# Optimization experiments

Hardware: AMD Instinct MI355X
Metric: run time of the kernel (lower is better)

The kernel has to match this reference:

```python
import jax, jax.numpy as jnp
import numpy as np

B, T, C_IN, H, W = 4, 3, 64, 64, 64
E = 96            # embed_dim
K = 3             # patch_size / deformable kernel size
PAD = 1
N = K * K         # 9 sampled positions per pixel
TOPK = 2
DG = 8            # deformable groups


def conv3x3(x, w, b):
    y = jax.lax.conv_general_dilated(x, w, (1, 1), ((1, 1), (1, 1)),
                                     dimension_numbers=('NCHW', 'OIHW', 'NCHW'))
    return y + b[None, :, None, None]


def lrelu(x):
    return jnp.where(x >= 0, x, 0.1 * x)


def deform_sample(x, off_feat, om_w, om_b):
    """DSP_sep2: modulated deformable sampling. Returns (B, C, N, H, W)."""
    B_, C, H_, W_ = x.shape
    om = conv3x3(off_feat, om_w, om_b).reshape(B_, 3, DG, N, H_, W_)
    off_y, off_x, mask = om[:, 0], om[:, 1], jax.nn.sigmoid(om[:, 2])  # (B,DG,N,H,W)
    ky = (jnp.arange(N) // K - PAD).astype(x.dtype)
    kx = (jnp.arange(N) % K - PAD).astype(x.dtype)
    py = off_y + ky[None, None, :, None, None] + jnp.arange(H_, dtype=x.dtype)[None, None, None, :, None]
    px = off_x + kx[None, None, :, None, None] + jnp.arange(W_, dtype=x.dtype)[None, None, None, None, :]
    y0 = jnp.floor(py); x0 = jnp.floor(px)
    wy = py - y0;       wx = px - x0
    xg = x.reshape(B_, DG, C // DG, H_, W_)
    gat = jax.vmap(jax.vmap(lambda xg_, yi, xi: xg_[:, yi, xi]))  # -> (B,DG,Cg,N,H,W)

    def corner(yc, xc, wgt):
        valid = ((yc >= 0) & (yc < H_) & (xc >= 0) & (xc < W_)).astype(x.dtype)
        yi = jnp.clip(yc, 0, H_ - 1).astype(jnp.int32)
        xi = jnp.clip(xc, 0, W_ - 1).astype(jnp.int32)
        return gat(xg, yi, xi) * (wgt * valid)[:, :, None]

    out = (corner(y0,     x0,     (1 - wy) * (1 - wx)) +
           corner(y0,     x0 + 1, (1 - wy) * wx) +
           corner(y0 + 1, x0,     wy * (1 - wx)) +
           corner(y0 + 1, x0 + 1, wy * wx))
    out = out * mask[:, :, None]  # modulation
    return out.reshape(B_, C, N, H_, W_)


def deform_attn(q, k, v, oc1_w, oc1_b, oc2_w, oc2_b, om_w, om_b):
    B_, E_, H_, W_ = q.shape
    HW = H_ * W_
    off = lrelu(conv3x3(jnp.concatenate([q, k], axis=1), oc1_w, oc1_b))
    off = lrelu(conv3x3(off, oc2_w, oc2_b))
    ko = deform_sample(k, off, om_w, om_b).transpose(0, 3, 4, 2, 1).reshape(B_, HW, N, E_)
    vo = deform_sample(v, off, om_w, om_b).transpose(0, 3, 4, 2, 1).reshape(B_, HW, N, E_)
    qr = q.reshape(B_, E_, HW).transpose(0, 2, 1)              # (B,HW,E)
    rel = jnp.einsum('bpne,bpe->bpn', ko, qr)                  # (B,HW,N)
    vals, idx = jax.lax.top_k(rel, TOPK)                       # (B,HW,k)
    corr = jax.nn.softmax(vals, axis=-1)
    idx_e = jnp.broadcast_to(idx[..., None], idx.shape + (E_,))
    ksel = jnp.take_along_axis(ko, idx_e, axis=2)              # (B,HW,k,E)
    vsel = jnp.take_along_axis(vo, idx_e, axis=2)
    k_up = jnp.einsum('bpke,bpk->bpe', ksel, corr)
    w_ori = jnp.einsum('bpe,bpe->bp', qr, k_up)                # (B,HW)
    v_re = jnp.einsum('bpke,bpk->bpe', vsel, corr).transpose(0, 2, 1)  # (B,E,HW)
    return w_ori, v_re


def setup_inputs() -> dict:
    key = jax.random.key(0)
    ks = jax.random.split(key, 18)
    s = 0.05
    return {
        'fea_full_map': jax.random.normal(ks[0], (B, T, C_IN, H, W), jnp.float32),
        'cf_w': s * jax.random.normal(ks[1], (E, C_IN, 3, 3), jnp.float32),
        'cf_b': s * jax.random.normal(ks[2], (E,), jnp.float32),
        'wq':   s * jax.random.normal(ks[3], (E, E), jnp.float32),
        'bq':   s * jax.random.normal(ks[4], (E,), jnp.float32),
        'wk':   s * jax.random.normal(ks[5], (E, E), jnp.float32),
        'bk':   s * jax.random.normal(ks[6], (E,), jnp.float32),
        'wv':   s * jax.random.normal(ks[7], (E, E), jnp.float32),
        'bv':   s * jax.random.normal(ks[8], (E,), jnp.float32),
        'oc1_w': s * jax.random.normal(ks[9], (E, 2 * E, 3, 3), jnp.float32),
        'oc1_b': s * jax.random.normal(ks[10], (E,), jnp.float32),
        'oc2_w': s * jax.random.normal(ks[11], (E, E, 3, 3), jnp.float32),
        'oc2_b': s * jax.random.normal(ks[12], (E,), jnp.float32),
        'om_w': 0.01 * jax.random.normal(ks[13], (DG * 3 * N, E, 3, 3), jnp.float32),
        'om_b': 0.01 * jax.random.normal(ks[14], (DG * 3 * N,), jnp.float32),
        'cl_w': s * jax.random.normal(ks[15], (C_IN, E, 3, 3), jnp.float32),
        'cl_b': s * jax.random.normal(ks[16], (C_IN,), jnp.float32),
    }


def reference(fea_full_map, cf_w, cf_b, wq, bq, wk, bk, wv, bv,
              oc1_w, oc1_b, oc2_w, oc2_b, om_w, om_b, cl_w, cl_b):
    B_, T_, C_, H_, W_ = fea_full_map.shape
    x = fea_full_map.reshape(B_ * T_, C_, H_, W_)
    emb = conv3x3(x, cf_w, cf_b).reshape(B_, T_, E, H_, W_)
    # per-frame linear Q/K/V over the channel dim (nn.Linear: y = x W^T + b)
    q = jnp.einsum('btchw,dc->btdhw', emb, wq) + bq[None, None, :, None, None]
    k = jnp.einsum('btchw,dc->btdhw', emb, wk) + bk[None, None, :, None, None]
    v = jnp.einsum('btchw,dc->btdhw', emb, wv) + bv[None, None, :, None, None]
    feats = []
    for jj in range(T_):
        ws, vs = [], []
        for ii in range(T_):
            if ii != jj:
                w_, v_ = deform_attn(q[:, jj], k[:, ii], v[:, ii],
                                     oc1_w, oc1_b, oc2_w, oc2_b, om_w, om_b)
                ws.append(w_); vs.append(v_)
        wm = jax.nn.softmax(jnp.stack(ws, axis=1), axis=1)  # (B, T-1, HW)
        vm = jnp.stack(vs, axis=1)                          # (B, T-1, E, HW)
        feats.append((vm * wm[:, :, None, :]).sum(axis=1).reshape(B_, E, H_, W_))
    f = jnp.stack(feats, axis=1).reshape(B_ * T_, E, H_, W_)
    out = conv3x3(f, cl_w, cl_b)
    return out + x
```

## Files before the change

kernel.cpp:

```cpp
#include <hip/hip_runtime.h>
#include <math.h>

#define PIXN 4096

typedef _Float16 f16;
typedef short s16x8 __attribute__((ext_vector_type(8)));
typedef unsigned short u16x4 __attribute__((ext_vector_type(4)));
typedef float f32x4 __attribute__((ext_vector_type(4)));

__device__ __forceinline__ f16 f2h(float f) { return (f16)f; }
__device__ __forceinline__ float h2f(f16 h) { return (float)h; }

__device__ __forceinline__ unsigned short f2bf(float f) {
  unsigned u = __float_as_uint(f);
  u += 0x7fffu + ((u >> 16) & 1u);
  return (unsigned short)(u >> 16);
}
__device__ __forceinline__ float bf2f(unsigned short h) {
  return __uint_as_float(((unsigned)h) << 16);
}

enum { ACT_NONE = 0, ACT_LRELU = 1, ACT_SIG144 = 2 };
enum { IN_FLAT = 1, IN_UVPAIR = 2, IN_QKV = 3, IN_BF = 4, IN_MERGE = 5 };
enum { OUT_FLAT = 0, OUT_NCHWRES = 1, OUT_BF = 2 };

__device__ __forceinline__ void wprep_mfma(const float* __restrict__ w, unsigned short* __restrict__ dst,
                                           int srcCIN, int cinOff, int COUTv, int COUTP,
                                           int total, int idx) {
  if (idx >= total) return;
  int e = idx & 7;
  int t = idx >> 3;
  int co = t % COUTP; t /= COUTP;
  int kch = t & 3; t >>= 2;
  int kc = t % 3;
  int tap = t / 3;
  int ci = kc * 32 + kch * 8 + e;
  float v = 0.f;
  if (co < COUTv) v = w[((long)co * srcCIN + cinOff + ci) * 9 + tap];
  unsigned short h = f2bf(v);
  dst[idx] = h;
  dst[total + idx] = f2bf(v - bf2f(h));
}

__global__ __launch_bounds__(256) void prep_all(
    const float* __restrict__ cf_w, const float* __restrict__ oc1_w,
    const float* __restrict__ oc2_w, const float* __restrict__ om_w,
    const float* __restrict__ cl_w,
    const float* __restrict__ wq, const float* __restrict__ wk, const float* __restrict__ wv,
    const float* __restrict__ bq, const float* __restrict__ bk, const float* __restrict__ bv,
    const float* __restrict__ cf_b,
    unsigned short* __restrict__ WBQ, float* __restrict__ BQ,
    unsigned short* __restrict__ WB1, unsigned short* __restrict__ WB2,
    unsigned short* __restrict__ WB3, unsigned short* __restrict__ WB4) {
  int idx = blockIdx.x * 256 + threadIdx.x;
  switch (blockIdx.y) {
    case 0: {
      if (idx < 288) {
        int m = idx / 96, ep = idx % 96;
        const float* wm = (m == 0) ? wq : (m == 1) ? wk : wv;
        const float* bm = (m == 0) ? bq : (m == 1) ? bk : bv;
        float s = bm[ep];
        for (int c = 0; c < 96; ++c) s = fmaf(wm[ep * 96 + c], cf_b[c], s);
        BQ[idx] = s;
      }
      if (idx < 165888) {
        int e = idx & 7;
        int t = idx >> 3;
        int co = t % 288; t /= 288;
        int kch = t & 3; t >>= 2;
        int kc = t & 1, tap = t >> 1;
        int ci = kc * 32 + kch * 8 + e;
        int m = co / 96, ep = co % 96;
        const float* wm = (m == 0) ? wq : (m == 1) ? wk : wv;
        float s = 0.f;
        for (int c = 0; c < 96; ++c)
          s = fmaf(wm[ep * 96 + c], cf_w[((long)c * 64 + ci) * 9 + tap], s);
        unsigned short h = f2bf(s);
        WBQ[idx] = h;
        WBQ[165888 + idx] = f2bf(s - bf2f(h));
      }
      break;
    }
    case 1: wprep_mfma(oc1_w, WB1, 192, 0, 96, 96, 82944, idx); break;
    case 2: wprep_mfma(oc1_w, WB1 + 2 * 82944, 192, 96, 96, 96, 82944, idx); break;
    case 3: wprep_mfma(oc2_w, WB2, 96, 0, 96, 96, 82944, idx); break;
    case 4: wprep_mfma(om_w, WB3, 96, 0, 216, 256, 221184, idx); break;
    default: wprep_mfma(cl_w, WB4, 96, 0, 64, 64, 55296, idx); break;
  }
}

__global__ __launch_bounds__(256) void nchw2bf(const float* __restrict__ fea,
                                               unsigned short* __restrict__ hi,
                                               unsigned short* __restrict__ lo) {
  const int y = blockIdx.x;
  const int img = blockIdx.y;
  const int t = threadIdx.x;
  const int x = t & 63, cg = t >> 6;
  __shared__ unsigned short sh[64][68], sl[64][68];
  const float* base = fea + ((long)img * 64) * PIXN + y * 64;
#pragma unroll
  for (int k = 0; k < 16; ++k) {
    int ci = cg * 16 + k;
    float v = base[(long)ci * PIXN + x];
    unsigned short h = f2bf(v);
    sh[x][ci] = h;
    sl[x][ci] = f2bf(v - bf2f(h));
  }
  __syncthreads();
  const long ob = (long)img * PIXN + y * 64;
  for (int i = t; i < 2048; i += 256) {
    int plane = i >> 10;
    int r = i & 1023;
    int px = r >> 4, q4 = r & 15;
    u16x4 v4 = *reinterpret_cast<const u16x4*>(plane ? &sl[px][q4 * 4] : &sh[px][q4 * 4]);
    unsigned short* dst = (plane ? lo : hi) + (ob + px) * 64 + q4 * 4;
    *reinterpret_cast<u16x4*>(dst) = v4;
  }
}

template <int CIN, int COUT, int COUTW, int NCOG, int IMODE, int ACT, int OMODE, int WN>
__global__ __launch_bounds__(512, 4) void conv3x3r(
    const float* __restrict__ in, const float* __restrict__ in2,
    const float* __restrict__ bias_in,
    const unsigned short* __restrict__ WB,
    const float* __restrict__ bias,
    float* __restrict__ out,
    const float* __restrict__ resid) {
  constexpr int KC = CIN / 32;
  constexpr int WM = 8 / WN;
  constexpr int MT = WN;
  constexpr int COG = COUTW / NCOG;
  constexpr int NTW = COG / (WN * 16);
  constexpr int AST = 4 * 66 * 8 + 8;
  constexpr int APL = 4 * AST;
  constexpr int BSTEP = COUTW * 32;
  constexpr int TOTB = 9 * KC * BSTEP;

  __shared__ __align__(16) unsigned short Abuf[2 * APL];
  __shared__ float s_sm[(IMODE == IN_MERGE) ? 528 : 4];

  const int tid = threadIdx.x;
  const int lane = tid & 63;
  const int wid = tid >> 6;
  const int wm = wid % WM;
  const int wn = wid / WM;
  const int iz = blockIdx.y;
  const int y0 = blockIdx.x * 2;
  const int zoff = (NCOG > 1) ? blockIdx.z * COG : 0;

  const float* baseA = nullptr;
  const float* baseB2 = nullptr;
  const unsigned short* hpl = nullptr;
  const unsigned short* lpl = nullptr;
  const unsigned short* wbe = WB;
  int LDV = CIN;
  if constexpr (IMODE == IN_UVPAIR) {
    int pair = iz >> 2, b = iz & 3;
    int jj = pair >> 1, rr2 = pair & 1;
    int ii = (rr2 == 0) ? (jj == 0 ? 1 : 0) : (jj == 2 ? 1 : 2);
    baseA = in + (long)(b * 3 + jj) * (PIXN * 96);
    baseB2 = in2 + (long)(b * 3 + ii) * (PIXN * 96);
    LDV = 96;
  } else if constexpr (IMODE == IN_QKV) {
    int sel = iz / 12, img = iz % 12;
    baseA = in + (long)img * (PIXN * 288) + sel * 96;
    wbe = WB + (long)sel * (2 * TOTB);
    LDV = 288;
  } else if constexpr (IMODE == IN_BF) {
    hpl = reinterpret_cast<const unsigned short*>(in) + (long)iz * ((long)PIXN * CIN);
    lpl = reinterpret_cast<const unsigned short*>(in2) + (long)iz * ((long)PIXN * CIN);
  } else if constexpr (IMODE == IN_MERGE) {
  } else {
    baseA = in + (long)iz * ((long)PIXN * CIN);
    LDV = CIN;
  }

  auto stageA = [&](int kc) {
    if constexpr (IMODE == IN_BF) {
      for (int i = tid; i < 4 * 66 * 4; i += 512) {
        int ci8 = i & 3;
        int t = i >> 2;
        int xp = t % 66, rr = t / 66;
        int y = y0 + rr - 1, x = xp - 1;
        s16x8 hv = {0, 0, 0, 0, 0, 0, 0, 0};
        s16x8 lv = {0, 0, 0, 0, 0, 0, 0, 0};
        if ((unsigned)y < 64u && (unsigned)x < 64u) {
          long off = (long)(y * 64 + x) * CIN + kc * 32 + ci8 * 8;
          hv = *reinterpret_cast<const s16x8*>(hpl + off);
          lv = *reinterpret_cast<const s16x8*>(lpl + off);
        }
        int base = ci8 * AST + (rr * 66 + xp) * 8;
        *reinterpret_cast<s16x8*>(&Abuf[base]) = hv;
        *reinterpret_cast<s16x8*>(&Abuf[APL + base]) = lv;
      }
    } else if constexpr (IMODE == IN_MERGE) {
      const f16* vrep = reinterpret_cast<const f16*>(in);
      const int bb = iz / 3, jjm = iz % 3;
      const int pr0 = jjm * 2;
      for (int i = tid; i < 4 * 66 * 8; i += 512) {
        int ci4 = i & 7;
        int t = i >> 3;
        int xp = t % 66, rr = t / 66;
        int y = y0 + rr - 1, x = xp - 1;
        float4 v = make_float4(0.f, 0.f, 0.f, 0.f);
        if ((unsigned)y < 64u && (unsigned)x < 64u) {
          long bpi = (long)bb * PIXN + y * 64 + x;
          float s0 = s_sm[t * 2], s1 = s_sm[t * 2 + 1];
          const f16* pa = vrep + ((long)pr0 * 16384 + bpi) * 96 + kc * 32 + ci4 * 4;
          const f16* pb = vrep + ((long)(pr0 + 1) * 16384 + bpi) * 96 + kc * 32 + ci4 * 4;
          v.x = s0 * h2f(pa[0]) + s1 * h2f(pb[0]);
          v.y = s0 * h2f(pa[1]) + s1 * h2f(pb[1]);
          v.z = s0 * h2f(pa[2]) + s1 * h2f(pb[2]);
          v.w = s0 * h2f(pa[3]) + s1 * h2f(pb[3]);
        }
        unsigned short h0 = f2bf(v.x), h1 = f2bf(v.y), h2 = f2bf(v.z), h3 = f2bf(v.w);
        u16x4 hv = {h0, h1, h2, h3};
        u16x4 lv = {f2bf(v.x - bf2f(h0)), f2bf(v.y - bf2f(h1)),
                    f2bf(v.z - bf2f(h2)), f2bf(v.w - bf2f(h3))};
        int base = (ci4 >> 1) * AST + (rr * 66 + xp) * 8 + (ci4 & 1) * 4;
        *reinterpret_cast<u16x4*>(&Abuf[base]) = hv;
        *reinterpret_cast<u16x4*>(&Abuf[APL + base]) = lv;
      }
    } else {
      for (int i = tid; i < 4 * 66 * 8; i += 512) {
        int ci4 = i & 7;
        int t = i >> 3;
        int xp = t % 66, rr = t / 66;
        int y = y0 + rr - 1, x = xp - 1;
        float4 v = make_float4(0.f, 0.f, 0.f, 0.f);
        if ((unsigned)y < 64u && (unsigned)x < 64u) {
          long off = (long)(y * 64 + x) * LDV + kc * 32 + ci4 * 4;
          if constexpr (IMODE == IN_UVPAIR) {
            float4 u = *reinterpret_cast<const float4*>(baseA + off);
            float4 w2 = *reinterpret_cast<const float4*>(baseB2 + off);
            float4 bi = *reinterpret_cast<const float4*>(bias_in + kc * 32 + ci4 * 4);
            v.x = u.x + w2.x + bi.x; v.x = v.x >= 0.f ? v.x : 0.1f * v.x;
            v.y = u.y + w2.y + bi.y; v.y = v.y >= 0.f ? v.y : 0.1f * v.y;
            v.z = u.z + w2.z + bi.z; v.z = v.z >= 0.f ? v.z : 0.1f * v.z;
            v.w = u.w + w2.w + bi.w; v.w = v.w >= 0.f ? v.w : 0.1f * v.w;
          } else {
            v = *reinterpret_cast<const float4*>(baseA + off);
          }
        }
        unsigned short h0 = f2bf(v.x), h1 = f2bf(v.y), h2 = f2bf(v.z), h3 = f2bf(v.w);
        u16x4 hv = {h0, h1, h2, h3};
        u16x4 lv = {f2bf(v.x - bf2f(h0)), f2bf(v.y - bf2f(h1)),
                    f2bf(v.z - bf2f(h2)), f2bf(v.w - bf2f(h3))};
        int base = (ci4 >> 1) * AST + (rr * 66 + xp) * 8 + (ci4 & 1) * 4;
        *reinterpret_cast<u16x4*>(&Abuf[base]) = hv;
        *reinterpret_cast<u16x4*>(&Abuf[APL + base]) = lv;
      }
    }
  };

  f32x4 acc[MT][NTW];
#pragma unroll
  for (int nt = 0; nt < NTW; ++nt) {
    int co = zoff + (wn * NTW + nt) * 16 + (lane & 15);
    float b0 = 0.f;
    if (bias != nullptr && co < COUT) b0 = bias[co];
#pragma unroll
    for (int mt = 0; mt < MT; ++mt) {
      acc[mt][nt][0] = b0; acc[mt][nt][1] = b0;
      acc[mt][nt][2] = b0; acc[mt][nt][3] = b0;
    }
  }

  if constexpr (IMODE == IN_MERGE) {
    const float* wbp = in2;
    const int bb = iz / 3, jjm = iz % 3;
    const int pr0 = jjm * 2;
    for (int t = tid; t < 264; t += 512) {
      int rr = t / 66, xp = t - rr * 66;
      int y = y0 + rr - 1, x = xp - 1;
      float s0 = 0.f, s1 = 0.f;
      if ((unsigned)y < 64u && (unsigned)x < 64u) {
        long bpi = (long)bb * PIXN + y * 64 + x;
        float w0 = wbp[(long)pr0 * 16384 + bpi];
        float w1 = wbp[(long)(pr0 + 1) * 16384 + bpi];
        float mx = fmaxf(w0, w1);
        float e0 = expf(w0 - mx), e1 = expf(w1 - mx);
        float inv = 1.f / (e0 + e1);
        s0 = e0 * inv; s1 = e1 * inv;
      }
      s_sm[t * 2] = s0; s_sm[t * 2 + 1] = s1;
    }
    __syncthreads();
  }

  stageA(0);
  __syncthreads();

  const int blo = ((lane >> 4) * COUTW + zoff + (wn * NTW) * 16 + (lane & 15)) * 8;

  s16x8 cbh[NTW], cbl[NTW], pbh[NTW], pbl[NTW];
#pragma unroll
  for (int nt = 0; nt < NTW; ++nt) {
    const unsigned short* p = wbe + (long)nt * 128 + blo;
    pbh[nt] = *reinterpret_cast<const s16x8*>(p);
    pbl[nt] = *reinterpret_cast<const s16x8*>(p + TOTB);
  }

  long bo = 0;
#pragma unroll 1
  for (int kc = 0; kc < KC; ++kc) {
#pragma unroll 1
    for (int tap = 0; tap < 9; ++tap) {
      const int dy = tap / 3, dx = tap % 3;
      const bool last = (kc == KC - 1) && (tap == 8);
      const long bo_next = (tap < 8) ? bo + (long)KC * BSTEP : (long)(kc + 1) * BSTEP;

#pragma unroll
      for (int nt = 0; nt < NTW; ++nt) { cbh[nt] = pbh[nt]; cbl[nt] = pbl[nt]; }
      if (!last) {
#pragma unroll
        for (int nt = 0; nt < NTW; ++nt) {
          const unsigned short* np = wbe + bo_next + (long)nt * 128 + blo;
          pbh[nt] = *reinterpret_cast<const s16x8*>(np);
          pbl[nt] = *reinterpret_cast<const s16x8*>(np + TOTB);
        }
      }

      s16x8 ah[MT], al[MT];
      {
        int ci8 = lane >> 4;
        int m = lane & 15;
#pragma unroll
        for (int mt = 0; mt < MT; ++mt) {
          int px = (wm * MT + mt) * 16 + m;
          int r = px >> 6, x = px & 63;
          int aoff = ci8 * AST + ((r + dy) * 66 + (x + dx)) * 8;
          ah[mt] = *reinterpret_cast<const s16x8*>(&Abuf[aoff]);
          al[mt] = *reinterpret_cast<const s16x8*>(&Abuf[APL + aoff]);
        }
      }

#pragma unroll
      for (int nt = 0; nt < NTW; ++nt) {
#pragma unroll
        for (int mt = 0; mt < MT; ++mt) {
          acc[mt][nt] = __builtin_amdgcn_mfma_f32_16x16x32_bf16(ah[mt], cbh[nt], acc[mt][nt], 0, 0, 0);
          acc[mt][nt] = __builtin_amdgcn_mfma_f32_16x16x32_bf16(al[mt], cbh[nt], acc[mt][nt], 0, 0, 0);
          acc[mt][nt] = __builtin_amdgcn_mfma_f32_16x16x32_bf16(ah[mt], cbl[nt], acc[mt][nt], 0, 0, 0);
        }
      }
      bo = bo_next;
    }
    if (kc + 1 < KC) {
      __syncthreads();
      stageA(kc + 1);
      __syncthreads();
    }
  }

#pragma unroll
  for (int mt = 0; mt < MT; ++mt) {
#pragma unroll
    for (int nt = 0; nt < NTW; ++nt) {
      int co = zoff + (wn * NTW + nt) * 16 + (lane & 15);
      if (COUTW > COUT && co >= COUT) continue;
#pragma unroll
      for (int r = 0; r < 4; ++r) {
        int px = (wm * MT + mt) * 16 + (lane >> 4) * 4 + r;
        float v = acc[mt][nt][r];
        if constexpr (ACT == ACT_LRELU) v = v >= 0.f ? v : 0.1f * v;
        if constexpr (ACT == ACT_SIG144) {
          if (co >= 144) v = 1.f / (1.f + expf(-v));
        }
        if constexpr (OMODE == OUT_FLAT) {
          const long obase = (long)iz * PIXN + blockIdx.x * 128;
          out[(obase + px) * COUT + co] = v;
        } else if constexpr (OMODE == OUT_BF) {
          unsigned short* outh = reinterpret_cast<unsigned short*>(out);
          const long plane = (long)gridDim.y * PIXN * COUT;
          const long obase = (long)iz * PIXN + blockIdx.x * 128;
          long oidx = (obase + px) * COUT + co;
          unsigned short h = f2bf(v);
          outh[oidx] = h;
          outh[plane + oidx] = f2bf(v - bf2f(h));
        } else {
          long oo = (long)iz * ((long)COUT * PIXN) + (long)co * PIXN + blockIdx.x * 128 + px;
          out[oo] = v + resid[oo];
        }
      }
    }
  }
}

#define CWSLOT 580
__global__ __launch_bounds__(256) void attn3_k(const float* __restrict__ qkv,
                                               const float* __restrict__ om,
                                               float* __restrict__ w_buf,
                                               f16* __restrict__ vre) {
  const int pair = blockIdx.y;
  const int jj = pair >> 1, rr = pair & 1;
  const int ii = (rr == 0) ? (jj == 0 ? 1 : 0) : (jj == 2 ? 1 : 2);
  const int wv = threadIdx.x >> 6;
  const int lane = threadIdx.x & 63;
  const int bp0 = blockIdx.x * 8 + wv * 2;

  __shared__ float s_om[8 * 216];
  __shared__ float s_cw[8 * CWSLOT];

  {
    const float* omrow = om + ((long)pair * 16384 + bp0) * 216;
    float* dst = s_om + wv * 432;
    for (int i = lane; i < 432; i += 64) dst[i] = omrow[i];
  }
  __syncthreads();

  for (int t = lane; t < 144; t += 64) {
    int ph = t / 72, cmb = t - ph * 72;
    int g = cmb / 9, n = cmb - g * 9;
    int p = (bp0 + ph) & 4095;
    int y = p >> 6, x = p & 63;
    const float* so = s_om + (wv * 2 + ph) * 216;
    float oy = so[g * 9 + n], ox = so[72 + g * 9 + n], m = so[144 + g * 9 + n];
    float py = oy + (float)(y + n / 3 - 1);
    float px = ox + (float)(x + n % 3 - 1);
    float y0f = floorf(py), x0f = floorf(px);
    float wy = py - y0f, wx = px - x0f;
    float* dst = s_cw + (wv * 2 + ph) * CWSLOT + cmb * 8;
#pragma unroll
    for (int dy = 0; dy < 2; ++dy) {
#pragma unroll
      for (int dx = 0; dx < 2; ++dx) {
        float yc = y0f + dy, xc = x0f + dx;
        bool valid = (yc >= 0.f) & (yc < 64.f) & (xc >= 0.f) & (xc < 64.f);
        float w = (dy ? wy : 1.f - wy) * (dx ? wx : 1.f - wx) * m;
        w = valid ? w : 0.f;
        int yi = (int)fminf(fmaxf(yc, 0.f), 63.f);
        int xi = (int)fminf(fmaxf(xc, 0.f), 63.f);
        int idx = (yi * 64 + xi) * 288 + 96;
        dst[dy * 2 + dx] = w;
        dst[4 + dy * 2 + dx] = __int_as_float(idx);
      }
    }
  }
  __syncthreads();

  const int ph = lane >> 5;
  const int li = lane & 31;
  const int bp = bp0 + ph;
  const int b = bp >> 12;
  const int cb = li * 3;
  const int g = li >> 2;
  const float* kimg = qkv + (long)(b * 3 + ii) * (PIXN * 288);
  const float* qrow = qkv + ((long)(b * 3 + jj) * PIXN + (bp & 4095)) * 288 + cb;
  const float q0 = qrow[0], q1 = qrow[1], q2 = qrow[2];
  const float* cw = s_cw + (wv * 2 + ph) * CWSLOT + g * 9 * 8;

  float ka[9][3];
  float rel[9];
#pragma unroll
  for (int n = 0; n < 9; ++n) {
    float4 w4 = *reinterpret_cast<const float4*>(cw + n * 8);
    float4 i4 = *reinterpret_cast<const float4*>(cw + n * 8 + 4);
    int ia = __float_as_int(i4.x) + cb, ib = __float_as_int(i4.y) + cb;
    int ic = __float_as_int(i4.z) + cb, id = __float_as_int(i4.w) + cb;
#pragma unroll
    for (int j = 0; j < 3; ++j) {
      float a = w4.x * kimg[ia + j];
      a = fmaf(w4.y, kimg[ib + j], a);
      a = fmaf(w4.z, kimg[ic + j], a);
      a = fmaf(w4.w, kimg[id + j], a);
      ka[n][j] = a;
    }
    float part = q0 * ka[n][0];
    part = fmaf(q1, ka[n][1], part);
    part = fmaf(q2, ka[n][2], part);
#pragma unroll
    for (int off = 16; off > 0; off >>= 1) part += __shfl_xor(part, off, 64);
    rel[n] = part;
  }

  int i0 = 0; float v0 = rel[0];
  float ks0a = ka[0][0], ks0b = ka[0][1], ks0c = ka[0][2];
#pragma unroll
  for (int n = 1; n < 9; ++n) {
    bool t = rel[n] > v0;
    v0 = t ? rel[n] : v0; i0 = t ? n : i0;
    ks0a = t ? ka[n][0] : ks0a; ks0b = t ? ka[n][1] : ks0b; ks0c = t ? ka[n][2] : ks0c;
  }
  int i1 = 0; float v1 = -3.4e38f;
  float ks1a = 0.f, ks1b = 0.f, ks1c = 0.f;
#pragma unroll
  for (int n = 0; n < 9; ++n) {
    bool t = (n != i0) && rel[n] > v1;
    v1 = t ? rel[n] : v1; i1 = t ? n : i1;
    ks1a = t ? ka[n][0] : ks1a; ks1b = t ? ka[n][1] : ks1b; ks1c = t ? ka[n][2] : ks1c;
  }
  float e = expf(v1 - v0);
  float cw0 = 1.f / (1.f + e), cw1 = e * cw0;

  float wpart = q0 * (cw0 * ks0a + cw1 * ks1a);
  wpart = fmaf(q1, cw0 * ks0b + cw1 * ks1b, wpart);
  wpart = fmaf(q2, cw0 * ks0c + cw1 * ks1c, wpart);
#pragma unroll
  for (int off = 16; off > 0; off >>= 1) wpart += __shfl_xor(wpart, off, 64);
  if (li == 0) w_buf[(long)pair * 16384 + bp] = wpart;

  float4 wA = *reinterpret_cast<const float4*>(cw + i0 * 8);
  float4 iA = *reinterpret_cast<const float4*>(cw + i0 * 8 + 4);
  float4 wB = *reinterpret_cast<const float4*>(cw + i1 * 8);
  float4 iB = *reinterpret_cast<const float4*>(cw + i1 * 8 + 4);
  int a0 = __float_as_int(iA.x) + 96 + cb, a1 = __float_as_int(iA.y) + 96 + cb;
  int a2 = __float_as_int(iA.z) + 96 + cb, a3 = __float_as_int(iA.w) + 96 + cb;
  int b0 = __float_as_int(iB.x) + 96 + cb, b1 = __float_as_int(iB.y) + 96 + cb;
  int b2 = __float_as_int(iB.z) + 96 + cb, b3 = __float_as_int(iB.w) + 96 + cb;
  f16* vrow = vre + ((long)pair * 16384 + bp) * 96 + cb;
#pragma unroll
  for (int j = 0; j < 3; ++j) {
    float va = wA.x * kimg[a0 + j];
    va = fmaf(wA.y, kimg[a1 + j], va);
    va = fmaf(wA.z, kimg[a2 + j], va);
    va = fmaf(wA.w, kimg[a3 + j], va);
    float vb = wB.x * kimg[b0 + j];
    vb = fmaf(wB.y, kimg[b1 + j], vb);
    vb = fmaf(wB.z, kimg[b2 + j], vb);
    vb = fmaf(wB.w, kimg[b3 + j], vb);
    vrow[j] = f2h(cw0 * va + cw1 * vb);
  }
}

extern "C" void kernel_launch(void* const* d_in, const int* in_sizes, int n_in,
                              void* d_out, int out_size, void* d_ws, size_t ws_size,
                              hipStream_t stream) {
  const float* fea = (const float*)d_in[0];
  const float* cf_w = (const float*)d_in[1];
  const float* cf_b = (const float*)d_in[2];
  const float* wq = (const float*)d_in[3];
  const float* bq = (const float*)d_in[4];
  const float* wk = (const float*)d_in[5];
  const float* bk = (const float*)d_in[6];
  const float* wv = (const float*)d_in[7];
  const float* bv = (const float*)d_in[8];
  const float* oc1_w = (const float*)d_in[9];
  const float* oc1_b = (const float*)d_in[10];
  const float* oc2_w = (const float*)d_in[11];
  const float* oc2_b = (const float*)d_in[12];
  const float* om_w = (const float*)d_in[13];
  const float* om_b = (const float*)d_in[14];
  const float* cl_w = (const float*)d_in[15];
  const float* cl_b = (const float*)d_in[16];

  char* base = (char*)d_ws;
  size_t o = 0;
  auto carve = [&](size_t bytes) { char* p = base + o; o += (bytes + 255) & ~255UL; return p; };

  unsigned short* WBQ = (unsigned short*)carve(2UL * 165888 * 2);
  float* BQ = (float*)carve(288UL * 4);
  unsigned short* WB1 = (unsigned short*)carve(2UL * 2 * 82944 * 2);
  unsigned short* WB2 = (unsigned short*)carve(2UL * 82944 * 2);
  unsigned short* WB3 = (unsigned short*)carve(2UL * 221184 * 2);
  unsigned short* WB4 = (unsigned short*)carve(2UL * 55296 * 2);
  unsigned short* feaH = (unsigned short*)carve(12UL * PIXN * 64 * 2);
  unsigned short* feaL = (unsigned short*)carve(12UL * PIXN * 64 * 2);

  float* om_t = (float*)carve(21233664UL * 4);
  float* qkv_t = (float*)carve(14155776UL * 4);
  float* U_t = (float*)carve(4718592UL * 4);
  float* V_t = (float*)carve(4718592UL * 4);
  unsigned short* off2B = (unsigned short*)carve(2UL * 9437184 * 2);
  float* w_buf = (float*)carve(98304UL * 4);
  f16* vre_b = (f16*)V_t;

  prep_all<<<dim3(864, 6), 256, 0, stream>>>(cf_w, oc1_w, oc2_w, om_w, cl_w,
                                             wq, wk, wv, bq, bk, bv, cf_b,
                                             WBQ, BQ, WB1, WB2, WB3, WB4);

  nchw2bf<<<dim3(64, 12), 256, 0, stream>>>(fea, feaH, feaL);

  conv3x3r<64, 288, 288, 3, IN_BF, ACT_NONE, OUT_FLAT, 2><<<dim3(32, 12, 3), 512, 0, stream>>>(
      (const float*)feaH, (const float*)feaL, nullptr, WBQ, BQ, qkv_t, nullptr);

  conv3x3r<96, 96, 96, 1, IN_QKV, ACT_NONE, OUT_FLAT, 2><<<dim3(32, 24, 1), 512, 0, stream>>>(
      qkv_t, nullptr, nullptr, WB1, nullptr, U_t, nullptr);

  conv3x3r<96, 96, 96, 1, IN_UVPAIR, ACT_LRELU, OUT_BF, 2><<<dim3(32, 24, 1), 512, 0, stream>>>(
      U_t, V_t, oc1_b, WB2, oc2_b, (float*)off2B, nullptr);

  conv3x3r<96, 216, 256, 2, IN_BF, ACT_SIG144, OUT_FLAT, 4><<<dim3(32, 24, 2), 512, 0, stream>>>(
      (const float*)off2B, (const float*)(off2B + 9437184), nullptr, WB3, om_b, om_t, nullptr);

  attn3_k<<<dim3(2048, 6), 256, 0, stream>>>(qkv_t, om_t, w_buf, vre_b);

  conv3x3r<96, 64, 64, 1, IN_MERGE, ACT_NONE, OUT_NCHWRES, 2><<<dim3(32, 12, 1), 512, 0, stream>>>(
      (const float*)vre_b, w_buf, nullptr, WB4, cl_b, (float*)d_out, fea);
}
```

Before: 501.5 us.

## Interleave bf16 hi/lo split planes per pixel and swizzle attention block order

The hi and lo bf16 split planes were stored as two separate tensors. They are now interleaved per pixel in 32-channel chunks, so the conv staging loads for both halves come from nearby addresses and the producer writes go to one record. This applies to the nchw2bf output and the OUT_BF epilogue that feeds the om conv. The attention kernel's block index is also remapped so that consecutive blocks touch strided pixel regions, which changes the cache and locality pattern. Both changes alter memory access patterns across several kernels and could hurt coalescing if the new strides interact badly.

```diff
diff --git a/kernel.cpp b/kernel.cpp
--- a/kernel.cpp
+++ b/kernel.cpp
@@ -90,8 +90,7 @@
 }
 
 __global__ __launch_bounds__(256) void nchw2bf(const float* __restrict__ fea,
-                                               unsigned short* __restrict__ hi,
-                                               unsigned short* __restrict__ lo) {
+                                               unsigned short* __restrict__ bf) {
   const int y = blockIdx.x;
   const int img = blockIdx.y;
   const int t = threadIdx.x;
@@ -113,8 +112,8 @@
     int r = i & 1023;
     int px = r >> 4, q4 = r & 15;
     u16x4 v4 = *reinterpret_cast<const u16x4*>(plane ? &sl[px][q4 * 4] : &sh[px][q4 * 4]);
-    unsigned short* dst = (plane ? lo : hi) + (ob + px) * 64 + q4 * 4;
-    *reinterpret_cast<u16x4*>(dst) = v4;
+    long dst = (ob + px) * 128 + (q4 >> 3) * 64 + plane * 32 + (q4 & 7) * 4;
+    *reinterpret_cast<u16x4*>(bf + dst) = v4;
   }
 }
 
@@ -151,7 +150,6 @@
   const float* baseA = nullptr;
   const float* baseB2 = nullptr;
   const unsigned short* hpl = nullptr;
-  const unsigned short* lpl = nullptr;
   const unsigned short* wbe = WB;
   int LDV = CIN;
   if constexpr (IMODE == IN_UVPAIR) {
@@ -167,8 +165,7 @@
     wbe = WB + (long)sel * (2 * TOTB);
     LDV = 288;
   } else if constexpr (IMODE == IN_BF) {
-    hpl = reinterpret_cast<const unsigned short*>(in) + (long)iz * ((long)PIXN * CIN);
-    lpl = reinterpret_cast<const unsigned short*>(in2) + (long)iz * ((long)PIXN * CIN);
+    hpl = reinterpret_cast<const unsigned short*>(in) + (long)iz * ((long)PIXN * CIN * 2);
   } else if constexpr (IMODE == IN_MERGE) {
   } else {
     baseA = in + (long)iz * ((long)PIXN * CIN);
@@ -185,9 +182,9 @@
         s16x8 hv = {0, 0, 0, 0, 0, 0, 0, 0};
         s16x8 lv = {0, 0, 0, 0, 0, 0, 0, 0};
         if ((unsigned)y < 64u && (unsigned)x < 64u) {
-          long off = (long)(y * 64 + x) * CIN + kc * 32 + ci8 * 8;
+          long off = (long)(y * 64 + x) * (CIN * 2) + kc * 64 + ci8 * 8;
           hv = *reinterpret_cast<const s16x8*>(hpl + off);
-          lv = *reinterpret_cast<const s16x8*>(lpl + off);
+          lv = *reinterpret_cast<const s16x8*>(hpl + off + 32);
         }
         int base = ci8 * AST + (rr * 66 + xp) * 8;
         *reinterpret_cast<s16x8*>(&Abuf[base]) = hv;
@@ -372,12 +369,11 @@
           out[(obase + px) * COUT + co] = v;
         } else if constexpr (OMODE == OUT_BF) {
           unsigned short* outh = reinterpret_cast<unsigned short*>(out);
-          const long plane = (long)gridDim.y * PIXN * COUT;
-          const long obase = (long)iz * PIXN + blockIdx.x * 128;
-          long oidx = (obase + px) * COUT + co;
+          long prow = (long)iz * PIXN + blockIdx.x * 128 + px;
+          long rec = prow * (COUT * 2) + (co >> 5) * 64 + (co & 31);
           unsigned short h = f2bf(v);
-          outh[oidx] = h;
-          outh[plane + oidx] = f2bf(v - bf2f(h));
+          outh[rec] = h;
+          outh[rec + 32] = f2bf(v - bf2f(h));
         } else {
           long oo = (long)iz * ((long)COUT * PIXN) + (long)co * PIXN + blockIdx.x * 128 + px;
           out[oo] = v + resid[oo];
@@ -397,7 +393,8 @@
   const int ii = (rr == 0) ? (jj == 0 ? 1 : 0) : (jj == 2 ? 1 : 2);
   const int wv = threadIdx.x >> 6;
   const int lane = threadIdx.x & 63;
-  const int bp0 = blockIdx.x * 8 + wv * 2;
+  const int xs = (blockIdx.x & 7) * 256 + (blockIdx.x >> 3);
+  const int bp0 = xs * 8 + wv * 2;
 
   __shared__ float s_om[8 * 216];
   __shared__ float s_cw[8 * CWSLOT];
@@ -554,14 +551,13 @@
   unsigned short* WB2 = (unsigned short*)carve(2UL * 82944 * 2);
   unsigned short* WB3 = (unsigned short*)carve(2UL * 221184 * 2);
   unsigned short* WB4 = (unsigned short*)carve(2UL * 55296 * 2);
-  unsigned short* feaH = (unsigned short*)carve(12UL * PIXN * 64 * 2);
-  unsigned short* feaL = (unsigned short*)carve(12UL * PIXN * 64 * 2);
+  unsigned short* feaB = (unsigned short*)carve(12UL * PIXN * 128 * 2);
 
   float* om_t = (float*)carve(21233664UL * 4);
   float* qkv_t = (float*)carve(14155776UL * 4);
   float* U_t = (float*)carve(4718592UL * 4);
   float* V_t = (float*)carve(4718592UL * 4);
-  unsigned short* off2B = (unsigned short*)carve(2UL * 9437184 * 2);
+  unsigned short* off2B = (unsigned short*)carve(24UL * PIXN * 192 * 2);
   float* w_buf = (float*)carve(98304UL * 4);
   f16* vre_b = (f16*)V_t;
 
@@ -569,10 +565,10 @@
                                              wq, wk, wv, bq, bk, bv, cf_b,
                                              WBQ, BQ, WB1, WB2, WB3, WB4);
 
-  nchw2bf<<<dim3(64, 12), 256, 0, stream>>>(fea, feaH, feaL);
+  nchw2bf<<<dim3(64, 12), 256, 0, stream>>>(fea, feaB);
 
   conv3x3r<64, 288, 288, 3, IN_BF, ACT_NONE, OUT_FLAT, 2><<<dim3(32, 12, 3), 512, 0, stream>>>(
-      (const float*)feaH, (const float*)feaL, nullptr, WBQ, BQ, qkv_t, nullptr);
+      (const float*)feaB, nullptr, nullptr, WBQ, BQ, qkv_t, nullptr);
 
   conv3x3r<96, 96, 96, 1, IN_QKV, ACT_NONE, OUT_FLAT, 2><<<dim3(32, 24, 1), 512, 0, stream>>>(
       qkv_t, nullptr, nullptr, WB1, nullptr, U_t, nullptr);
@@ -581,7 +577,7 @@
       U_t, V_t, oc1_b, WB2, oc2_b, (float*)off2B, nullptr);
 
   conv3x3r<96, 216, 256, 2, IN_BF, ACT_SIG144, OUT_FLAT, 4><<<dim3(32, 24, 2), 512, 0, stream>>>(
-      (const float*)off2B, (const float*)(off2B + 9437184), nullptr, WB3, om_b, om_t, nullptr);
+      (const float*)off2B, nullptr, nullptr, WB3, om_b, om_t, nullptr);
 
   attn3_k<<<dim3(2048, 6), 256, 0, stream>>>(qkv_t, om_t, w_buf, vre_b);
 
```

New measurement: 501.1 us. Within noise of the previous version (-0.1%).
